# Performance work log

Measured on AMD Instinct MI355X. Metric: run time of the kernel, lower is better.

Reference implementation:

```python
import jax, jax.numpy as jnp
import numpy as np

N = 4096
E = 262144
IN_C = 128
OUT_C = 128
EDGE_D = 16


def setup_inputs() -> dict:
    key = jax.random.key(0)
    k = jax.random.split(key, 8)
    x = jax.random.normal(k[0], (N, IN_C), dtype=jnp.float32)
    edge_index = jax.random.randint(k[1], (2, E), 0, N, dtype=jnp.int64)
    edge_attr = jax.random.normal(k[2], (N, N, EDGE_D), dtype=jnp.float32)
    # nn.Linear params: y = x @ W.T + b; store pre-transposed W for x @ W
    s1 = 1.0 / np.sqrt(IN_C + EDGE_D)
    s2 = 1.0 / np.sqrt(OUT_C)
    W1 = jax.random.uniform(k[3], (IN_C + EDGE_D, OUT_C), jnp.float32, -s1, s1)
    b1 = jax.random.uniform(k[4], (OUT_C,), jnp.float32, -s1, s1)
    W2 = jax.random.uniform(k[5], (OUT_C, OUT_C), jnp.float32, -s2, s2)
    b2 = jax.random.uniform(k[6], (OUT_C,), jnp.float32, -s2, s2)
    return {"x": x, "edge_index": edge_index, "edge_attr": edge_attr,
            "W1": W1, "b1": b1, "W2": W2, "b2": b2}


def reference(x, edge_index, edge_attr, W1, b1, W2, b2):
    row, col = edge_index[0], edge_index[1]
    x_row = x[row]                      # [E, IN_C] gather
    e = edge_attr[row, col]             # [E, EDGE_D] gather from dense NxN table
    h = jnp.concatenate([x_row, e], axis=-1)     # [E, IN_C+EDGE_D]
    h = jax.nn.relu(h @ W1 + b1)                  # [E, OUT_C]
    h = jax.nn.relu(h @ W2 + b2)                  # [E, OUT_C]
    # global_add_pool(out, col): scatter-add edges into node buckets by col
    return jax.ops.segment_sum(h, col, num_segments=x.shape[0])  # [N, OUT_C]
```

## Files before the change

kernel.cpp:

```cpp
#include <hip/hip_runtime.h>
#include <hip/hip_bf16.h>

#define NN 4096
#define IC 128
#define OC 128
#define ED 16
#define EPB 64
#define NT 256
#define NSLOT 16
#define NBLK 512
#define NCPY 8

typedef __bf16 bf16x8 __attribute__((ext_vector_type(8)));
typedef float  f32x16 __attribute__((ext_vector_type(16)));

#define BAR() do { asm volatile("s_waitcnt lgkmcnt(0)" ::: "memory"); \
    __builtin_amdgcn_s_barrier(); \
    __builtin_amdgcn_sched_barrier(0); } while (0)

__device__ __forceinline__ unsigned short bf16u(float f) {
    unsigned int u = __float_as_uint(f);
    u = (u + 0x7FFFu + ((u >> 16) & 1u)) >> 16;
    return (unsigned short)u;
}
__device__ __forceinline__ float bf16tof(unsigned short h) {
    return __uint_as_float(((unsigned int)h) << 16);
}
__device__ __forceinline__ int swzk(int row) { return (row ^ (row >> 3)) & 7; }

__global__ __launch_bounds__(128) void k_xw1(
    const float* __restrict__ x, const float* __restrict__ W1,
    const float* __restrict__ b1, const int* __restrict__ eidx,
    float* __restrict__ xw1b, float* __restrict__ out,
    int* __restrict__ hist8, int E)
{
    __shared__ float xs[8][IC];
    const int t = threadIdx.x;
    const int r0 = blockIdx.x * 8;
    #pragma unroll
    for (int r = 0; r < 8; ++r) xs[r][t] = x[(size_t)(r0 + r) * IC + t];

    const float4 z = make_float4(0.f, 0.f, 0.f, 0.f);
    float4* o4 = (float4*)out;
    o4[blockIdx.x * 256 + t]       = z;
    o4[blockIdx.x * 256 + 128 + t] = z;

    {
        const int e0 = blockIdx.x * 512;
        #pragma unroll
        for (int j = 0; j < 4; ++j) {
            const int k = (2 * blockIdx.x + (j >> 1)) & (NCPY - 1);
            atomicAdd(&hist8[k * 4096 + eidx[E + e0 + t + j * 128]], 1);
        }
    }

    __syncthreads();
    float acc[8];
    const float bb = b1[t];
    #pragma unroll
    for (int r = 0; r < 8; ++r) acc[r] = bb;
    #pragma unroll 4
    for (int k = 0; k < IC; ++k) {
        const float w = W1[(size_t)k * OC + t];
        #pragma unroll
        for (int r = 0; r < 8; ++r) acc[r] = fmaf(xs[r][k], w, acc[r]);
    }
    #pragma unroll
    for (int r = 0; r < 8; ++r) xw1b[(size_t)(r0 + r) * OC + t] = acc[r];
}

__global__ __launch_bounds__(256) void k_scanA(
    const int* __restrict__ hist8, int* __restrict__ binloc,
    int* __restrict__ blocksum)
{
    __shared__ int sb[256];
    const int t = threadIdx.x;
    const int bin = blockIdx.x * 256 + t;
    int s = 0;
    #pragma unroll
    for (int k = 0; k < NCPY; ++k) s += hist8[k * 4096 + bin];
    sb[t] = s;
    __syncthreads();
    if (t == 0) {
        int a = 0;
        for (int i = 0; i < 256; ++i) { const int v = sb[i]; sb[i] = a; a += v; }
        blocksum[blockIdx.x] = a;
    }
    __syncthreads();
    binloc[bin] = sb[t];
}

__global__ __launch_bounds__(256) void k_scanB(
    const int* __restrict__ hist8, const int* __restrict__ binloc,
    const int* __restrict__ blocksum, int* __restrict__ cursor8,
    int* __restrict__ colstart, int E)
{
    __shared__ int baseL;
    const int t = threadIdx.x;
    if (t == 0) {
        int a = 0;
        for (int j = 0; j < (int)blockIdx.x; ++j) a += blocksum[j];
        baseL = a;
    }
    __syncthreads();
    const int bin = blockIdx.x * 256 + t;
    int off = baseL + binloc[bin];
    colstart[bin] = off;
    #pragma unroll
    for (int k = 0; k < NCPY; ++k) {
        cursor8[k * 4096 + bin] = off;
        off += hist8[k * 4096 + bin];
    }
    if (bin == 4095) colstart[4096] = E;
}

__global__ void k_scatter(const int* __restrict__ eidx, int* __restrict__ cursor8,
                          int2* __restrict__ csr, int E) {
    const int i = blockIdx.x * blockDim.x + threadIdx.x;
    const int k = blockIdx.x & (NCPY - 1);
    if (i < E) {
        const int row = eidx[i];
        const int col = eidx[E + i];
        const int pos = atomicAdd(&cursor8[k * 4096 + col], 1);
        csr[pos] = make_int2(row, col);
    }
}

__global__ __launch_bounds__(NT, 2) void k_edge10(
    const int2* __restrict__ csr, const float* __restrict__ eattr,
    const float* __restrict__ xw1b, const float* __restrict__ W1,
    const float* __restrict__ W2, const float* __restrict__ b2,
    const int* __restrict__ colstart, float* __restrict__ out, int E)
{
    extern __shared__ char smem[];
    char*   const h1hi = smem;
    char*   const h1lo = smem + 16384;
    float4* const eaL  = (float4*)(smem + 32768);
    float4* const w1L  = (float4*)(smem + 40960);
    float*  const lacc = (float*)(smem + 49152);
    int*    const srowL = (int*)(smem + 57344);
    int*    const scolL = srowL + 256;

    const int t   = threadIdx.x;
    const int l   = t & 63;
    const int wid = t >> 6;
    const int cg  = t & 15, eg = t >> 4;
    const int c0  = cg << 3, e0 = eg << 2;
    const int sz  = (eg >> 1) & 3;
    const int em  = t >> 2, q = t & 3;
    const int esz = (em >> 3) & 3;

    const int lm  = l & 31;
    const int hi  = l >> 5;
    const int c2  = wid * 32 + lm;

    w1L[t]       = ((const float4*)(W1 + (size_t)IC * OC))[t];
    w1L[t + NT]  = ((const float4*)(W1 + (size_t)IC * OC))[t + NT];

    bf16x8 w2h[8], w2l[8];
    #pragma unroll
    for (int s = 0; s < 8; ++s) {
        union { unsigned short us[8]; bf16x8 v; } Uh, Ul;
        #pragma unroll
        for (int j = 0; j < 8; ++j) {
            const float w = W2[(size_t)(s * 16 + hi * 8 + j) * OC + c2];
            const unsigned short h = bf16u(w);
            Uh.us[j] = h;
            Ul.us[j] = bf16u(w - bf16tof(h));
        }
        w2h[s] = Uh.v; w2l[s] = Ul.v;
    }
    const float b2s = b2[c2];

    #pragma unroll
    for (int i = 0; i < NSLOT * OC / NT; ++i) lacc[t + NT * i] = 0.f;

    const int nper = (E / EPB) / NBLK;
    const int ibb  = blockIdx.x * nper;

    if (t < EPB) {
        const int2 r0v = csr[(size_t)ibb * EPB + t];
        srowL[t] = r0v.x; scolL[t] = r0v.y;
        const int ib1 = (nper > 1) ? 1 : 0;
        const int2 r1v = csr[(size_t)(ibb + ib1) * EPB + t];
        srowL[64 + t] = r1v.x; scolL[64 + t] = r1v.y;
    }
    __syncthreads();
    const int colbase0 = scolL[0];

    float4 pA;
    {
        const int r = srowL[em], c = scolL[em];
        pA = ((const float4*)(eattr + ((size_t)r * NN + c) * ED))[q];
    }
    eaL[(em * 4 + q) ^ esz] = pA;
    float4 xa[4], xb[4];
    #pragma unroll
    for (int ri = 0; ri < 4; ++ri) {
        const int row = srowL[e0 + ri];
        const float4* p = (const float4*)(xw1b + (size_t)row * OC + c0);
        xa[ri] = p[0]; xb[ri] = p[1];
    }
    int2 pidx;
    {
        const int ib2 = (nper > 2) ? 2 : (nper - 1);
        pidx = (t < EPB) ? csr[(size_t)(ibb + ib2) * EPB + t] : make_int2(0, 0);
    }
    __syncthreads();

    for (int ii = 0; ii < nper; ++ii) {
        const int cb  = ii & 1;
        const int ib4 = ii & 3;

        float4 ha[4], hb[4];
        #pragma unroll
        for (int ri = 0; ri < 4; ++ri) { ha[ri] = xa[ri]; hb[ri] = xb[ri]; }
        #pragma unroll
        for (int dc = 0; dc < 4; ++dc) {
            float4 ev[4];
            #pragma unroll
            for (int ri = 0; ri < 4; ++ri)
                ev[ri] = eaL[cb * 256 + ((((e0 + ri) * 4 + dc)) ^ sz)];
            #pragma unroll
            for (int dd = 0; dd < 4; ++dd) {
                const int d = dc * 4 + dd;
                const float4 wA = w1L[d * 32 + cg * 2];
                const float4 wB = w1L[d * 32 + cg * 2 + 1];
                #pragma unroll
                for (int ri = 0; ri < 4; ++ri) {
                    const float evd = (dd == 0) ? ev[ri].x : (dd == 1) ? ev[ri].y
                                     : (dd == 2) ? ev[ri].z : ev[ri].w;
                    ha[ri].x = fmaf(evd, wA.x, ha[ri].x);
                    ha[ri].y = fmaf(evd, wA.y, ha[ri].y);
                    ha[ri].z = fmaf(evd, wA.z, ha[ri].z);
                    ha[ri].w = fmaf(evd, wA.w, ha[ri].w);
                    hb[ri].x = fmaf(evd, wB.x, hb[ri].x);
                    hb[ri].y = fmaf(evd, wB.y, hb[ri].y);
                    hb[ri].z = fmaf(evd, wB.z, hb[ri].z);
                    hb[ri].w = fmaf(evd, wB.w, hb[ri].w);
                }
            }
        }
        #pragma unroll
        for (int ri = 0; ri < 4; ++ri) {
            const int row = e0 + ri;
            float v[8] = { ha[ri].x, ha[ri].y, ha[ri].z, ha[ri].w,
                           hb[ri].x, hb[ri].y, hb[ri].z, hb[ri].w };
            union { unsigned short us[8]; uint4 qv; } Hh, Hl;
            #pragma unroll
            for (int j = 0; j < 8; ++j) {
                const float f = fmaxf(v[j], 0.f);
                const unsigned short h = bf16u(f);
                Hh.us[j] = h;
                Hl.us[j] = bf16u(f - bf16tof(h));
            }
            const int boff = (cg * 16) ^ (swzk(row) << 4);
            *(uint4*)(h1hi + row * 256 + boff) = Hh.qv;
            *(uint4*)(h1lo + row * 256 + boff) = Hl.qv;
        }
        if (t < EPB) {
            srowL[((ii + 2) & 3) * 64 + t] = pidx.x;
            scolL[((ii + 2) & 3) * 64 + t] = pidx.y;
        }
        {
            const int jn = (ii + 1) & 3;
            const int r = srowL[jn * 64 + em], c = scolL[jn * 64 + em];
            pA = ((const float4*)(eattr + ((size_t)r * NN + c) * ED))[q];
            #pragma unroll
            for (int ri = 0; ri < 4; ++ri) {
                const int row = srowL[jn * 64 + e0 + ri];
                const float4* p = (const float4*)(xw1b + (size_t)row * OC + c0);
                xa[ri] = p[0]; xb[ri] = p[1];
            }
        }
        {
            const int iin = (ii + 3 < nper) ? (ii + 3) : (nper - 1);
            pidx = (t < EPB) ? csr[(size_t)(ibb + iin) * EPB + t] : make_int2(0, 0);
        }
        BAR();

        f32x16 acc0 = (f32x16)(0.0f);
        f32x16 acc1 = (f32x16)(0.0f);
        const int arow0 = lm;
        const int arow1 = 32 + lm;
        const int ak0 = swzk(arow0) << 4;
        const int ak1 = swzk(arow1) << 4;
        #pragma unroll
        for (int s = 0; s < 8; ++s) {
            const int kb = s * 32 + hi * 16;
            const bf16x8 aH0 = *(const bf16x8*)(h1hi + arow0 * 256 + (kb ^ ak0));
            const bf16x8 aL0 = *(const bf16x8*)(h1lo + arow0 * 256 + (kb ^ ak0));
            const bf16x8 aH1 = *(const bf16x8*)(h1hi + arow1 * 256 + (kb ^ ak1));
            const bf16x8 aL1 = *(const bf16x8*)(h1lo + arow1 * 256 + (kb ^ ak1));
            acc0 = __builtin_amdgcn_mfma_f32_32x32x16_bf16(aH0, w2h[s], acc0, 0, 0, 0);
            acc1 = __builtin_amdgcn_mfma_f32_32x32x16_bf16(aH1, w2h[s], acc1, 0, 0, 0);
            acc0 = __builtin_amdgcn_mfma_f32_32x32x16_bf16(aL0, w2h[s], acc0, 0, 0, 0);
            acc1 = __builtin_amdgcn_mfma_f32_32x32x16_bf16(aL1, w2h[s], acc1, 0, 0, 0);
            acc0 = __builtin_amdgcn_mfma_f32_32x32x16_bf16(aH0, w2l[s], acc0, 0, 0, 0);
            acc1 = __builtin_amdgcn_mfma_f32_32x32x16_bf16(aH1, w2l[s], acc1, 0, 0, 0);
        }

        #pragma unroll
        for (int p = 0; p < 2; ++p) {
            const int mbase = p * 32 + 4 * hi;
            #pragma unroll
            for (int g = 0; g < 4; ++g) {
                const int eb = mbase + 8 * g;
                float sv;
                {
                    const float a0 = (p == 0) ? acc0[4 * g] : acc1[4 * g];
                    sv = fmaxf(a0 + b2s, 0.f);
                }
                int ccur = scolL[ib4 * 64 + eb];
                #pragma unroll
                for (int j = 1; j < 4; ++j) {
                    const float aj = (p == 0) ? acc0[4 * g + j] : acc1[4 * g + j];
                    const float v = fmaxf(aj + b2s, 0.f);
                    const int c = scolL[ib4 * 64 + eb + j];
                    if (c == ccur) {
                        sv += v;
                    } else {
                        const int slot = ccur - colbase0;
                        if (slot < NSLOT) {
                            if (sv != 0.f) atomicAdd(&lacc[slot * OC + c2], sv);
                        } else {
                            if (sv != 0.f) atomicAdd(&out[(size_t)ccur * OC + c2], sv);
                        }
                        ccur = c; sv = v;
                    }
                }
                const int slot = ccur - colbase0;
                if (slot < NSLOT) {
                    if (sv != 0.f) atomicAdd(&lacc[slot * OC + c2], sv);
                } else {
                    if (sv != 0.f) atomicAdd(&out[(size_t)ccur * OC + c2], sv);
                }
            }
        }
        eaL[(cb ^ 1) * 256 + ((em * 4 + q) ^ esz)] = pA;
        BAR();
    }

    const int blk_e0 = ibb * EPB;
    const int blk_e1 = blk_e0 + nper * EPB;
    #pragma unroll 1
    for (int s = 0; s < NSLOT; ++s) {
        const int c = colbase0 + s;
        if (c >= NN) break;
        const int cs = colstart[c];
        const int ce = colstart[c + 1];
        if (ce <= blk_e0 || cs >= blk_e1) continue;
        if (t < OC) {
            const float v = lacc[s * OC + t];
            if (cs >= blk_e0 && ce <= blk_e1) {
                out[(size_t)c * OC + t] = v;
            } else if (v != 0.f) {
                atomicAdd(&out[(size_t)c * OC + t], v);
            }
        }
    }
}

#define LDS_BYTES 59392

extern "C" void kernel_launch(void* const* d_in, const int* in_sizes, int n_in,
                              void* d_out, int out_size, void* d_ws, size_t ws_size,
                              hipStream_t stream) {
    const float* x    = (const float*)d_in[0];
    const int*   eidx = (const int*)d_in[1];
    const float* ea   = (const float*)d_in[2];
    const float* W1   = (const float*)d_in[3];
    const float* b1   = (const float*)d_in[4];
    const float* W2   = (const float*)d_in[5];
    const float* b2   = (const float*)d_in[6];
    float* out = (float*)d_out;

    const int E = in_sizes[1] / 2;

    char* ws = (char*)d_ws;
    float* xw1b     = (float*)ws;
    int*   hist8    = (int*)(ws + 2097152);
    int*   cursor8  = (int*)(ws + 2097152 + 131072);
    int*   colstart = (int*)(ws + 2097152 + 262144);
    int*   binloc   = (int*)(ws + 2097152 + 294912);
    int*   blocksum = (int*)(ws + 2097152 + 311296);
    int2*  csr      = (int2*)(ws + 2097152 + 327680);

    hipMemsetAsync(hist8, 0, 131072, stream);
    k_xw1<<<NN / 8, 128, 0, stream>>>(x, W1, b1, eidx, xw1b, out, hist8, E);
    k_scanA<<<16, 256, 0, stream>>>(hist8, binloc, blocksum);
    k_scanB<<<16, 256, 0, stream>>>(hist8, binloc, blocksum, cursor8, colstart, E);
    k_scatter<<<(E + 255) / 256, 256, 0, stream>>>(eidx, cursor8, csr, E);

    hipFuncSetAttribute(reinterpret_cast<const void*>(k_edge10),
                        hipFuncAttributeMaxDynamicSharedMemorySize, LDS_BYTES);
    k_edge10<<<NBLK, NT, LDS_BYTES, stream>>>(csr, ea, xw1b, W1, W2, b2,
                                              colstart, out, E);
}
```

Baseline: 136.9 us.

## Halve edge tile and software-pipeline layer-1 one tile ahead of MFMA layer-2

The per-block edge tile shrinks from 64 to 32 edges, and the h1 LDS buffer is double-buffered. Layer 1 (edge-attr FMA plus bf16 split) for tile i+1 now runs before layer 2's MFMA for tile i, with gathers prefetched two tiles ahead. The aim is to overlap VALU work with MFMA and cut to one barrier per iteration. The trade-off is twice as many iterations with half the work each, and only half the threads issue the edge-attr gathers.

```diff
diff --git a/kernel.cpp b/kernel.cpp
--- a/kernel.cpp
+++ b/kernel.cpp
@@ -5,7 +5,7 @@
 #define IC 128
 #define OC 128
 #define ED 16
-#define EPB 64
+#define EPB 32
 #define NT 256
 #define NSLOT 16
 #define NBLK 512
@@ -126,7 +126,7 @@
     }
 }
 
-__global__ __launch_bounds__(NT, 2) void k_edge10(
+__global__ __launch_bounds__(NT, 2) void k_edge11(
     const int2* __restrict__ csr, const float* __restrict__ eattr,
     const float* __restrict__ xw1b, const float* __restrict__ W1,
     const float* __restrict__ W2, const float* __restrict__ b2,
@@ -136,26 +136,29 @@
     char*   const h1hi = smem;
     char*   const h1lo = smem + 16384;
     float4* const eaL  = (float4*)(smem + 32768);
-    float4* const w1L  = (float4*)(smem + 40960);
-    float*  const lacc = (float*)(smem + 49152);
-    int*    const srowL = (int*)(smem + 57344);
-    int*    const scolL = srowL + 256;
+    float4* const w1L  = (float4*)(smem + 36864);
+    float*  const lacc = (float*)(smem + 45056);
+    int*    const srowL = (int*)(smem + 53248);
+    int*    const scolL = srowL + 128;
 
     const int t   = threadIdx.x;
     const int l   = t & 63;
     const int wid = t >> 6;
     const int cg  = t & 15, eg = t >> 4;
-    const int c0  = cg << 3, e0 = eg << 2;
-    const int sz  = (eg >> 1) & 3;
+    const int c0  = cg << 3, e0 = eg << 1;
+    const int sz  = (eg >> 2) & 3;
     const int em  = t >> 2, q = t & 3;
     const int esz = (em >> 3) & 3;
+    const bool gth = (t < 128);
 
     const int lm  = l & 31;
     const int hi  = l >> 5;
     const int c2  = wid * 32 + lm;
-
-    w1L[t]       = ((const float4*)(W1 + (size_t)IC * OC))[t];
-    w1L[t + NT]  = ((const float4*)(W1 + (size_t)IC * OC))[t + NT];
+    const int arow = lm;
+    const int ak  = swzk(arow) << 4;
+
+    w1L[t]      = ((const float4*)(W1 + (size_t)IC * OC))[t];
+    w1L[t + NT] = ((const float4*)(W1 + (size_t)IC * OC))[t + NT];
 
     bf16x8 w2h[8], w2l[8];
     #pragma unroll
@@ -179,165 +182,169 @@
     const int ibb  = blockIdx.x * nper;
 
     if (t < EPB) {
-        const int2 r0v = csr[(size_t)ibb * EPB + t];
-        srowL[t] = r0v.x; scolL[t] = r0v.y;
-        const int ib1 = (nper > 1) ? 1 : 0;
-        const int2 r1v = csr[(size_t)(ibb + ib1) * EPB + t];
-        srowL[64 + t] = r1v.x; scolL[64 + t] = r1v.y;
+        #pragma unroll
+        for (int b = 0; b < 3; ++b) {
+            const int ib = (b < nper) ? b : (nper - 1);
+            const int2 rc = csr[(size_t)(ibb + ib) * EPB + t];
+            srowL[b * EPB + t] = rc.x;
+            scolL[b * EPB + t] = rc.y;
+        }
     }
     __syncthreads();
     const int colbase0 = scolL[0];
 
-    float4 pA;
-    {
+    float4 pA = make_float4(0.f, 0.f, 0.f, 0.f);
+    if (gth) {
         const int r = srowL[em], c = scolL[em];
         pA = ((const float4*)(eattr + ((size_t)r * NN + c) * ED))[q];
-    }
-    eaL[(em * 4 + q) ^ esz] = pA;
-    float4 xa[4], xb[4];
-    #pragma unroll
-    for (int ri = 0; ri < 4; ++ri) {
+        eaL[(em * 4 + q) ^ esz] = pA;
+    }
+    float4 xa[2], xb[2];
+    #pragma unroll
+    for (int ri = 0; ri < 2; ++ri) {
         const int row = srowL[e0 + ri];
         const float4* p = (const float4*)(xw1b + (size_t)row * OC + c0);
         xa[ri] = p[0]; xb[ri] = p[1];
     }
+    __syncthreads();
+
+    #define LAYER1(BUF) do { \
+        float4 ha[2], hb[2]; \
+        _Pragma("unroll") \
+        for (int ri = 0; ri < 2; ++ri) { ha[ri] = xa[ri]; hb[ri] = xb[ri]; } \
+        _Pragma("unroll") \
+        for (int dc = 0; dc < 4; ++dc) { \
+            float4 ev[2]; \
+            _Pragma("unroll") \
+            for (int ri = 0; ri < 2; ++ri) \
+                ev[ri] = eaL[(BUF) * 128 + (((e0 + ri) * 4 + dc) ^ sz)]; \
+            _Pragma("unroll") \
+            for (int dd = 0; dd < 4; ++dd) { \
+                const int d = dc * 4 + dd; \
+                const float4 wA = w1L[d * 32 + cg * 2]; \
+                const float4 wB = w1L[d * 32 + cg * 2 + 1]; \
+                _Pragma("unroll") \
+                for (int ri = 0; ri < 2; ++ri) { \
+                    const float evd = (dd == 0) ? ev[ri].x : (dd == 1) ? ev[ri].y \
+                                     : (dd == 2) ? ev[ri].z : ev[ri].w; \
+                    ha[ri].x = fmaf(evd, wA.x, ha[ri].x); \
+                    ha[ri].y = fmaf(evd, wA.y, ha[ri].y); \
+                    ha[ri].z = fmaf(evd, wA.z, ha[ri].z); \
+                    ha[ri].w = fmaf(evd, wA.w, ha[ri].w); \
+                    hb[ri].x = fmaf(evd, wB.x, hb[ri].x); \
+                    hb[ri].y = fmaf(evd, wB.y, hb[ri].y); \
+                    hb[ri].z = fmaf(evd, wB.z, hb[ri].z); \
+                    hb[ri].w = fmaf(evd, wB.w, hb[ri].w); \
+                } \
+            } \
+        } \
+        _Pragma("unroll") \
+        for (int ri = 0; ri < 2; ++ri) { \
+            const int row = e0 + ri; \
+            float v[8] = { ha[ri].x, ha[ri].y, ha[ri].z, ha[ri].w, \
+                           hb[ri].x, hb[ri].y, hb[ri].z, hb[ri].w }; \
+            union { unsigned short us[8]; uint4 qv; } Hh, Hl; \
+            _Pragma("unroll") \
+            for (int j = 0; j < 8; ++j) { \
+                const float f = fmaxf(v[j], 0.f); \
+                const unsigned short h = bf16u(f); \
+                Hh.us[j] = h; \
+                Hl.us[j] = bf16u(f - bf16tof(h)); \
+            } \
+            const int boff = (cg * 16) ^ (swzk(row) << 4); \
+            *(uint4*)(h1hi + (BUF) * 8192 + row * 256 + boff) = Hh.qv; \
+            *(uint4*)(h1lo + (BUF) * 8192 + row * 256 + boff) = Hl.qv; \
+        } \
+    } while (0)
+
+    LAYER1(0);
+
+    if (gth) {
+        const int r = srowL[1 * EPB + em], c = scolL[1 * EPB + em];
+        pA = ((const float4*)(eattr + ((size_t)r * NN + c) * ED))[q];
+    }
+    #pragma unroll
+    for (int ri = 0; ri < 2; ++ri) {
+        const int row = srowL[1 * EPB + e0 + ri];
+        const float4* p = (const float4*)(xw1b + (size_t)row * OC + c0);
+        xa[ri] = p[0]; xb[ri] = p[1];
+    }
     int2 pidx;
     {
-        const int ib2 = (nper > 2) ? 2 : (nper - 1);
-        pidx = (t < EPB) ? csr[(size_t)(ibb + ib2) * EPB + t] : make_int2(0, 0);
-    }
-    __syncthreads();
+        const int ib = (3 < nper) ? 3 : (nper - 1);
+        pidx = (t < EPB) ? csr[(size_t)(ibb + ib) * EPB + t] : make_int2(0, 0);
+    }
+    if (gth) eaL[1 * 128 + ((em * 4 + q) ^ esz)] = pA;
+    BAR();
 
     for (int ii = 0; ii < nper; ++ii) {
-        const int cb  = ii & 1;
+        const int cb2 = ii & 1;
+        const int nb  = (ii + 1) & 1;
         const int ib4 = ii & 3;
 
-        float4 ha[4], hb[4];
-        #pragma unroll
-        for (int ri = 0; ri < 4; ++ri) { ha[ri] = xa[ri]; hb[ri] = xb[ri]; }
-        #pragma unroll
-        for (int dc = 0; dc < 4; ++dc) {
-            float4 ev[4];
+        if (ii + 1 < nper) LAYER1(nb);
+
+        {
+            const int jb = (ii + 2) & 3;
+            if (gth) {
+                const int r = srowL[jb * EPB + em], c = scolL[jb * EPB + em];
+                pA = ((const float4*)(eattr + ((size_t)r * NN + c) * ED))[q];
+            }
             #pragma unroll
-            for (int ri = 0; ri < 4; ++ri)
-                ev[ri] = eaL[cb * 256 + ((((e0 + ri) * 4 + dc)) ^ sz)];
-            #pragma unroll
-            for (int dd = 0; dd < 4; ++dd) {
-                const int d = dc * 4 + dd;
-                const float4 wA = w1L[d * 32 + cg * 2];
-                const float4 wB = w1L[d * 32 + cg * 2 + 1];
-                #pragma unroll
-                for (int ri = 0; ri < 4; ++ri) {
-                    const float evd = (dd == 0) ? ev[ri].x : (dd == 1) ? ev[ri].y
-                                     : (dd == 2) ? ev[ri].z : ev[ri].w;
-                    ha[ri].x = fmaf(evd, wA.x, ha[ri].x);
-                    ha[ri].y = fmaf(evd, wA.y, ha[ri].y);
-                    ha[ri].z = fmaf(evd, wA.z, ha[ri].z);
-                    ha[ri].w = fmaf(evd, wA.w, ha[ri].w);
-                    hb[ri].x = fmaf(evd, wB.x, hb[ri].x);
-                    hb[ri].y = fmaf(evd, wB.y, hb[ri].y);
-                    hb[ri].z = fmaf(evd, wB.z, hb[ri].z);
-                    hb[ri].w = fmaf(evd, wB.w, hb[ri].w);
-                }
-            }
-        }
-        #pragma unroll
-        for (int ri = 0; ri < 4; ++ri) {
-            const int row = e0 + ri;
-            float v[8] = { ha[ri].x, ha[ri].y, ha[ri].z, ha[ri].w,
-                           hb[ri].x, hb[ri].y, hb[ri].z, hb[ri].w };
-            union { unsigned short us[8]; uint4 qv; } Hh, Hl;
-            #pragma unroll
-            for (int j = 0; j < 8; ++j) {
-                const float f = fmaxf(v[j], 0.f);
-                const unsigned short h = bf16u(f);
-                Hh.us[j] = h;
-                Hl.us[j] = bf16u(f - bf16tof(h));
-            }
-            const int boff = (cg * 16) ^ (swzk(row) << 4);
-            *(uint4*)(h1hi + row * 256 + boff) = Hh.qv;
-            *(uint4*)(h1lo + row * 256 + boff) = Hl.qv;
-        }
-        if (t < EPB) {
-            srowL[((ii + 2) & 3) * 64 + t] = pidx.x;
-            scolL[((ii + 2) & 3) * 64 + t] = pidx.y;
-        }
-        {
-            const int jn = (ii + 1) & 3;
-            const int r = srowL[jn * 64 + em], c = scolL[jn * 64 + em];
-            pA = ((const float4*)(eattr + ((size_t)r * NN + c) * ED))[q];
-            #pragma unroll
-            for (int ri = 0; ri < 4; ++ri) {
-                const int row = srowL[jn * 64 + e0 + ri];
+            for (int ri = 0; ri < 2; ++ri) {
+                const int row = srowL[jb * EPB + e0 + ri];
                 const float4* p = (const float4*)(xw1b + (size_t)row * OC + c0);
                 xa[ri] = p[0]; xb[ri] = p[1];
             }
         }
+        if (t < EPB) {
+            srowL[((ii + 3) & 3) * EPB + t] = pidx.x;
+            scolL[((ii + 3) & 3) * EPB + t] = pidx.y;
+        }
         {
-            const int iin = (ii + 3 < nper) ? (ii + 3) : (nper - 1);
-            pidx = (t < EPB) ? csr[(size_t)(ibb + iin) * EPB + t] : make_int2(0, 0);
-        }
-        BAR();
-
-        f32x16 acc0 = (f32x16)(0.0f);
-        f32x16 acc1 = (f32x16)(0.0f);
-        const int arow0 = lm;
-        const int arow1 = 32 + lm;
-        const int ak0 = swzk(arow0) << 4;
-        const int ak1 = swzk(arow1) << 4;
+            const int ib = (ii + 4 < nper) ? (ii + 4) : (nper - 1);
+            pidx = (t < EPB) ? csr[(size_t)(ibb + ib) * EPB + t] : make_int2(0, 0);
+        }
+
+        f32x16 acc = (f32x16)(0.0f);
         #pragma unroll
         for (int s = 0; s < 8; ++s) {
             const int kb = s * 32 + hi * 16;
-            const bf16x8 aH0 = *(const bf16x8*)(h1hi + arow0 * 256 + (kb ^ ak0));
-            const bf16x8 aL0 = *(const bf16x8*)(h1lo + arow0 * 256 + (kb ^ ak0));
-            const bf16x8 aH1 = *(const bf16x8*)(h1hi + arow1 * 256 + (kb ^ ak1));
-            const bf16x8 aL1 = *(const bf16x8*)(h1lo + arow1 * 256 + (kb ^ ak1));
-            acc0 = __builtin_amdgcn_mfma_f32_32x32x16_bf16(aH0, w2h[s], acc0, 0, 0, 0);
-            acc1 = __builtin_amdgcn_mfma_f32_32x32x16_bf16(aH1, w2h[s], acc1, 0, 0, 0);
-            acc0 = __builtin_amdgcn_mfma_f32_32x32x16_bf16(aL0, w2h[s], acc0, 0, 0, 0);
-            acc1 = __builtin_amdgcn_mfma_f32_32x32x16_bf16(aL1, w2h[s], acc1, 0, 0, 0);
-            acc0 = __builtin_amdgcn_mfma_f32_32x32x16_bf16(aH0, w2l[s], acc0, 0, 0, 0);
-            acc1 = __builtin_amdgcn_mfma_f32_32x32x16_bf16(aH1, w2l[s], acc1, 0, 0, 0);
-        }
-
-        #pragma unroll
-        for (int p = 0; p < 2; ++p) {
-            const int mbase = p * 32 + 4 * hi;
+            const bf16x8 aH = *(const bf16x8*)(h1hi + cb2 * 8192 + arow * 256 + (kb ^ ak));
+            const bf16x8 aL = *(const bf16x8*)(h1lo + cb2 * 8192 + arow * 256 + (kb ^ ak));
+            acc = __builtin_amdgcn_mfma_f32_32x32x16_bf16(aH, w2h[s], acc, 0, 0, 0);
+            acc = __builtin_amdgcn_mfma_f32_32x32x16_bf16(aL, w2h[s], acc, 0, 0, 0);
+            acc = __builtin_amdgcn_mfma_f32_32x32x16_bf16(aH, w2l[s], acc, 0, 0, 0);
+        }
+        #pragma unroll
+        for (int g = 0; g < 4; ++g) {
+            const int eb = 4 * hi + 8 * g;
+            float sv = fmaxf(acc[4 * g] + b2s, 0.f);
+            int ccur = scolL[ib4 * EPB + eb];
             #pragma unroll
-            for (int g = 0; g < 4; ++g) {
-                const int eb = mbase + 8 * g;
-                float sv;
-                {
-                    const float a0 = (p == 0) ? acc0[4 * g] : acc1[4 * g];
-                    sv = fmaxf(a0 + b2s, 0.f);
-                }
-                int ccur = scolL[ib4 * 64 + eb];
-                #pragma unroll
-                for (int j = 1; j < 4; ++j) {
-                    const float aj = (p == 0) ? acc0[4 * g + j] : acc1[4 * g + j];
-                    const float v = fmaxf(aj + b2s, 0.f);
-                    const int c = scolL[ib4 * 64 + eb + j];
-                    if (c == ccur) {
-                        sv += v;
+            for (int j = 1; j < 4; ++j) {
+                const float v = fmaxf(acc[4 * g + j] + b2s, 0.f);
+                const int c = scolL[ib4 * EPB + eb + j];
+                if (c == ccur) {
+                    sv += v;
+                } else {
+                    const int slot = ccur - colbase0;
+                    if (slot < NSLOT) {
+                        if (sv != 0.f) atomicAdd(&lacc[slot * OC + c2], sv);
                     } else {
-                        const int slot = ccur - colbase0;
-                        if (slot < NSLOT) {
-                            if (sv != 0.f) atomicAdd(&lacc[slot * OC + c2], sv);
-                        } else {
-                            if (sv != 0.f) atomicAdd(&out[(size_t)ccur * OC + c2], sv);
-                        }
-                        ccur = c; sv = v;
+                        if (sv != 0.f) atomicAdd(&out[(size_t)ccur * OC + c2], sv);
                     }
-                }
-                const int slot = ccur - colbase0;
-                if (slot < NSLOT) {
-                    if (sv != 0.f) atomicAdd(&lacc[slot * OC + c2], sv);
-                } else {
-                    if (sv != 0.f) atomicAdd(&out[(size_t)ccur * OC + c2], sv);
+                    ccur = c; sv = v;
                 }
             }
-        }
-        eaL[(cb ^ 1) * 256 + ((em * 4 + q) ^ esz)] = pA;
+            const int slot = ccur - colbase0;
+            if (slot < NSLOT) {
+                if (sv != 0.f) atomicAdd(&lacc[slot * OC + c2], sv);
+            } else {
+                if (sv != 0.f) atomicAdd(&out[(size_t)ccur * OC + c2], sv);
+            }
+        }
+        if (gth) eaL[cb2 * 128 + ((em * 4 + q) ^ esz)] = pA;
         BAR();
     }
 
@@ -359,9 +366,10 @@
             }
         }
     }
-}
-
-#define LDS_BYTES 59392
+    #undef LAYER1
+}
+
+#define LDS_BYTES 54272
 
 extern "C" void kernel_launch(void* const* d_in, const int* in_sizes, int n_in,
                               void* d_out, int out_size, void* d_ws, size_t ws_size,
@@ -392,8 +400,8 @@
     k_scanB<<<16, 256, 0, stream>>>(hist8, binloc, blocksum, cursor8, colstart, E);
     k_scatter<<<(E + 255) / 256, 256, 0, stream>>>(eidx, cursor8, csr, E);
 
-    hipFuncSetAttribute(reinterpret_cast<const void*>(k_edge10),
+    hipFuncSetAttribute(reinterpret_cast<const void*>(k_edge11),
                         hipFuncAttributeMaxDynamicSharedMemorySize, LDS_BYTES);
-    k_edge10<<<NBLK, NT, LDS_BYTES, stream>>>(csr, ea, xw1b, W1, W2, b2,
+    k_edge11<<<NBLK, NT, LDS_BYTES, stream>>>(csr, ea, xw1b, W1, W2, b2,
                                               colstart, out, E);
 }
```

Result: slower. 142.7 us (+4.3%).

## Compute edge-attribute part of first layer with split-bf16 MFMA instead of scalar FMA

Applied to the files above, without the earlier changes.

Replaces the scalar FP32 FMA loop that applied the 16-wide edge-attribute slice of W1 with three bf16 MFMA ops using a hi/lo split for near-FP32 accuracy. The xw1b gather is loaded straight into the MFMA accumulator layout, and edge attributes go directly to registers instead of through an LDS staging buffer. This drops the eaL and w1L LDS buffers, cutting LDS use and one staging step per tile. The cost is scalar per-element gathers of xw1b (16 per accumulator) and 2-byte scattered LDS stores of h1, which may raise memory-instruction count and bank conflicts.

```diff
diff --git a/kernel.cpp b/kernel.cpp
--- a/kernel.cpp
+++ b/kernel.cpp
@@ -126,7 +126,7 @@
     }
 }
 
-__global__ __launch_bounds__(NT, 2) void k_edge10(
+__global__ __launch_bounds__(NT, 2) void k_edge12(
     const int2* __restrict__ csr, const float* __restrict__ eattr,
     const float* __restrict__ xw1b, const float* __restrict__ W1,
     const float* __restrict__ W2, const float* __restrict__ b2,
@@ -135,27 +135,16 @@
     extern __shared__ char smem[];
     char*   const h1hi = smem;
     char*   const h1lo = smem + 16384;
-    float4* const eaL  = (float4*)(smem + 32768);
-    float4* const w1L  = (float4*)(smem + 40960);
-    float*  const lacc = (float*)(smem + 49152);
-    int*    const srowL = (int*)(smem + 57344);
+    float*  const lacc = (float*)(smem + 32768);
+    int*    const srowL = (int*)(smem + 40960);
     int*    const scolL = srowL + 256;
 
     const int t   = threadIdx.x;
     const int l   = t & 63;
     const int wid = t >> 6;
-    const int cg  = t & 15, eg = t >> 4;
-    const int c0  = cg << 3, e0 = eg << 2;
-    const int sz  = (eg >> 1) & 3;
-    const int em  = t >> 2, q = t & 3;
-    const int esz = (em >> 3) & 3;
-
     const int lm  = l & 31;
     const int hi  = l >> 5;
     const int c2  = wid * 32 + lm;
-
-    w1L[t]       = ((const float4*)(W1 + (size_t)IC * OC))[t];
-    w1L[t + NT]  = ((const float4*)(W1 + (size_t)IC * OC))[t + NT];
 
     bf16x8 w2h[8], w2l[8];
     #pragma unroll
@@ -169,6 +158,18 @@
             Ul.us[j] = bf16u(w - bf16tof(h));
         }
         w2h[s] = Uh.v; w2l[s] = Ul.v;
+    }
+    bf16x8 w1h, w1l;
+    {
+        union { unsigned short us[8]; bf16x8 v; } Uh, Ul;
+        #pragma unroll
+        for (int j = 0; j < 8; ++j) {
+            const float w = W1[(size_t)(IC + hi * 8 + j) * OC + c2];
+            const unsigned short h = bf16u(w);
+            Uh.us[j] = h;
+            Ul.us[j] = bf16u(w - bf16tof(h));
+        }
+        w1h = Uh.v; w1l = Ul.v;
     }
     const float b2s = b2[c2];
 
@@ -188,156 +189,153 @@
     __syncthreads();
     const int colbase0 = scolL[0];
 
-    float4 pA;
+    float4 pe0a, pe0b, pe1a, pe1b;
     {
-        const int r = srowL[em], c = scolL[em];
-        pA = ((const float4*)(eattr + ((size_t)r * NN + c) * ED))[q];
-    }
-    eaL[(em * 4 + q) ^ esz] = pA;
-    float4 xa[4], xb[4];
-    #pragma unroll
-    for (int ri = 0; ri < 4; ++ri) {
-        const int row = srowL[e0 + ri];
-        const float4* p = (const float4*)(xw1b + (size_t)row * OC + c0);
-        xa[ri] = p[0]; xb[ri] = p[1];
+        const int r0 = srowL[lm], cc0 = scolL[lm];
+        const float* p0 = eattr + ((size_t)r0 * NN + cc0) * ED + hi * 8;
+        pe0a = ((const float4*)p0)[0]; pe0b = ((const float4*)p0)[1];
+        const int r1 = srowL[32 + lm], cc1 = scolL[32 + lm];
+        const float* p1 = eattr + ((size_t)r1 * NN + cc1) * ED + hi * 8;
+        pe1a = ((const float4*)p1)[0]; pe1b = ((const float4*)p1)[1];
     }
     int2 pidx;
     {
         const int ib2 = (nper > 2) ? 2 : (nper - 1);
         pidx = (t < EPB) ? csr[(size_t)(ibb + ib2) * EPB + t] : make_int2(0, 0);
     }
-    __syncthreads();
 
     for (int ii = 0; ii < nper; ++ii) {
-        const int cb  = ii & 1;
         const int ib4 = ii & 3;
 
-        float4 ha[4], hb[4];
-        #pragma unroll
-        for (int ri = 0; ri < 4; ++ri) { ha[ri] = xa[ri]; hb[ri] = xb[ri]; }
-        #pragma unroll
-        for (int dc = 0; dc < 4; ++dc) {
-            float4 ev[4];
-            #pragma unroll
-            for (int ri = 0; ri < 4; ++ri)
-                ev[ri] = eaL[cb * 256 + ((((e0 + ri) * 4 + dc)) ^ sz)];
-            #pragma unroll
-            for (int dd = 0; dd < 4; ++dd) {
-                const int d = dc * 4 + dd;
-                const float4 wA = w1L[d * 32 + cg * 2];
-                const float4 wB = w1L[d * 32 + cg * 2 + 1];
-                #pragma unroll
-                for (int ri = 0; ri < 4; ++ri) {
-                    const float evd = (dd == 0) ? ev[ri].x : (dd == 1) ? ev[ri].y
-                                     : (dd == 2) ? ev[ri].z : ev[ri].w;
-                    ha[ri].x = fmaf(evd, wA.x, ha[ri].x);
-                    ha[ri].y = fmaf(evd, wA.y, ha[ri].y);
-                    ha[ri].z = fmaf(evd, wA.z, ha[ri].z);
-                    ha[ri].w = fmaf(evd, wA.w, ha[ri].w);
-                    hb[ri].x = fmaf(evd, wB.x, hb[ri].x);
-                    hb[ri].y = fmaf(evd, wB.y, hb[ri].y);
-                    hb[ri].z = fmaf(evd, wB.z, hb[ri].z);
-                    hb[ri].w = fmaf(evd, wB.w, hb[ri].w);
-                }
-            }
-        }
-        #pragma unroll
-        for (int ri = 0; ri < 4; ++ri) {
-            const int row = e0 + ri;
-            float v[8] = { ha[ri].x, ha[ri].y, ha[ri].z, ha[ri].w,
-                           hb[ri].x, hb[ri].y, hb[ri].z, hb[ri].w };
-            union { unsigned short us[8]; uint4 qv; } Hh, Hl;
+        bf16x8 ah0, al0, ah1, al1;
+        {
+            const float f0[8] = { pe0a.x, pe0a.y, pe0a.z, pe0a.w,
+                                  pe0b.x, pe0b.y, pe0b.z, pe0b.w };
+            const float f1[8] = { pe1a.x, pe1a.y, pe1a.z, pe1a.w,
+                                  pe1b.x, pe1b.y, pe1b.z, pe1b.w };
+            union { unsigned short us[8]; bf16x8 v; } H0, L0, H1, L1;
             #pragma unroll
             for (int j = 0; j < 8; ++j) {
-                const float f = fmaxf(v[j], 0.f);
+                unsigned short h = bf16u(f0[j]);
+                H0.us[j] = h; L0.us[j] = bf16u(f0[j] - bf16tof(h));
+                h = bf16u(f1[j]);
+                H1.us[j] = h; L1.us[j] = bf16u(f1[j] - bf16tof(h));
+            }
+            ah0 = H0.v; al0 = L0.v; ah1 = H1.v; al1 = L1.v;
+        }
+        f32x16 acc0, acc1;
+        #pragma unroll
+        for (int reg = 0; reg < 16; ++reg) {
+            const int r = (reg & 3) + 8 * (reg >> 2) + 4 * hi;
+            acc0[reg] = xw1b[(size_t)srowL[ib4 * 64 + r] * OC + c2];
+            acc1[reg] = xw1b[(size_t)srowL[ib4 * 64 + 32 + r] * OC + c2];
+        }
+        acc0 = __builtin_amdgcn_mfma_f32_32x32x16_bf16(ah0, w1h, acc0, 0, 0, 0);
+        acc1 = __builtin_amdgcn_mfma_f32_32x32x16_bf16(ah1, w1h, acc1, 0, 0, 0);
+        acc0 = __builtin_amdgcn_mfma_f32_32x32x16_bf16(al0, w1h, acc0, 0, 0, 0);
+        acc1 = __builtin_amdgcn_mfma_f32_32x32x16_bf16(al1, w1h, acc1, 0, 0, 0);
+        acc0 = __builtin_amdgcn_mfma_f32_32x32x16_bf16(ah0, w1l, acc0, 0, 0, 0);
+        acc1 = __builtin_amdgcn_mfma_f32_32x32x16_bf16(ah1, w1l, acc1, 0, 0, 0);
+        #pragma unroll
+        for (int reg = 0; reg < 16; ++reg) {
+            const int r = (reg & 3) + 8 * (reg >> 2) + 4 * hi;
+            {
+                const float f = fmaxf(acc0[reg], 0.f);
                 const unsigned short h = bf16u(f);
-                Hh.us[j] = h;
-                Hl.us[j] = bf16u(f - bf16tof(h));
-            }
-            const int boff = (cg * 16) ^ (swzk(row) << 4);
-            *(uint4*)(h1hi + row * 256 + boff) = Hh.qv;
-            *(uint4*)(h1lo + row * 256 + boff) = Hl.qv;
+                const unsigned short lo = bf16u(f - bf16tof(h));
+                const int byt = r * 256 + ((c2 * 2) ^ (swzk(r) << 4));
+                *(unsigned short*)(h1hi + byt) = h;
+                *(unsigned short*)(h1lo + byt) = lo;
+            }
+            {
+                const int r1 = r + 32;
+                const float f = fmaxf(acc1[reg], 0.f);
+                const unsigned short h = bf16u(f);
+                const unsigned short lo = bf16u(f - bf16tof(h));
+                const int byt = r1 * 256 + ((c2 * 2) ^ (swzk(r1) << 4));
+                *(unsigned short*)(h1hi + byt) = h;
+                *(unsigned short*)(h1lo + byt) = lo;
+            }
         }
         if (t < EPB) {
             srowL[((ii + 2) & 3) * 64 + t] = pidx.x;
             scolL[((ii + 2) & 3) * 64 + t] = pidx.y;
         }
         {
-            const int jn = (ii + 1) & 3;
-            const int r = srowL[jn * 64 + em], c = scolL[jn * 64 + em];
-            pA = ((const float4*)(eattr + ((size_t)r * NN + c) * ED))[q];
-            #pragma unroll
-            for (int ri = 0; ri < 4; ++ri) {
-                const int row = srowL[jn * 64 + e0 + ri];
-                const float4* p = (const float4*)(xw1b + (size_t)row * OC + c0);
-                xa[ri] = p[0]; xb[ri] = p[1];
-            }
-        }
-        {
             const int iin = (ii + 3 < nper) ? (ii + 3) : (nper - 1);
             pidx = (t < EPB) ? csr[(size_t)(ibb + iin) * EPB + t] : make_int2(0, 0);
         }
+        {
+            const int jb = (ii + 1) & 3;
+            const int r0 = srowL[jb * 64 + lm], cc0 = scolL[jb * 64 + lm];
+            const float* p0 = eattr + ((size_t)r0 * NN + cc0) * ED + hi * 8;
+            pe0a = ((const float4*)p0)[0]; pe0b = ((const float4*)p0)[1];
+            const int r1 = srowL[jb * 64 + 32 + lm], cc1 = scolL[jb * 64 + 32 + lm];
+            const float* p1 = eattr + ((size_t)r1 * NN + cc1) * ED + hi * 8;
+            pe1a = ((const float4*)p1)[0]; pe1b = ((const float4*)p1)[1];
+        }
         BAR();
 
-        f32x16 acc0 = (f32x16)(0.0f);
-        f32x16 acc1 = (f32x16)(0.0f);
-        const int arow0 = lm;
-        const int arow1 = 32 + lm;
-        const int ak0 = swzk(arow0) << 4;
-        const int ak1 = swzk(arow1) << 4;
-        #pragma unroll
-        for (int s = 0; s < 8; ++s) {
-            const int kb = s * 32 + hi * 16;
-            const bf16x8 aH0 = *(const bf16x8*)(h1hi + arow0 * 256 + (kb ^ ak0));
-            const bf16x8 aL0 = *(const bf16x8*)(h1lo + arow0 * 256 + (kb ^ ak0));
-            const bf16x8 aH1 = *(const bf16x8*)(h1hi + arow1 * 256 + (kb ^ ak1));
-            const bf16x8 aL1 = *(const bf16x8*)(h1lo + arow1 * 256 + (kb ^ ak1));
-            acc0 = __builtin_amdgcn_mfma_f32_32x32x16_bf16(aH0, w2h[s], acc0, 0, 0, 0);
-            acc1 = __builtin_amdgcn_mfma_f32_32x32x16_bf16(aH1, w2h[s], acc1, 0, 0, 0);
-            acc0 = __builtin_amdgcn_mfma_f32_32x32x16_bf16(aL0, w2h[s], acc0, 0, 0, 0);
-            acc1 = __builtin_amdgcn_mfma_f32_32x32x16_bf16(aL1, w2h[s], acc1, 0, 0, 0);
-            acc0 = __builtin_amdgcn_mfma_f32_32x32x16_bf16(aH0, w2l[s], acc0, 0, 0, 0);
-            acc1 = __builtin_amdgcn_mfma_f32_32x32x16_bf16(aH1, w2l[s], acc1, 0, 0, 0);
-        }
-
-        #pragma unroll
-        for (int p = 0; p < 2; ++p) {
-            const int mbase = p * 32 + 4 * hi;
+        {
+            f32x16 La0 = (f32x16)(0.0f);
+            f32x16 La1 = (f32x16)(0.0f);
+            const int arow0 = lm;
+            const int arow1 = 32 + lm;
+            const int ak0 = swzk(arow0) << 4;
+            const int ak1 = swzk(arow1) << 4;
             #pragma unroll
-            for (int g = 0; g < 4; ++g) {
-                const int eb = mbase + 8 * g;
-                float sv;
-                {
-                    const float a0 = (p == 0) ? acc0[4 * g] : acc1[4 * g];
-                    sv = fmaxf(a0 + b2s, 0.f);
-                }
-                int ccur = scolL[ib4 * 64 + eb];
+            for (int s = 0; s < 8; ++s) {
+                const int kb = s * 32 + hi * 16;
+                const bf16x8 aH0 = *(const bf16x8*)(h1hi + arow0 * 256 + (kb ^ ak0));
+                const bf16x8 aL0 = *(const bf16x8*)(h1lo + arow0 * 256 + (kb ^ ak0));
+                const bf16x8 aH1 = *(const bf16x8*)(h1hi + arow1 * 256 + (kb ^ ak1));
+                const bf16x8 aL1 = *(const bf16x8*)(h1lo + arow1 * 256 + (kb ^ ak1));
+                La0 = __builtin_amdgcn_mfma_f32_32x32x16_bf16(aH0, w2h[s], La0, 0, 0, 0);
+                La1 = __builtin_amdgcn_mfma_f32_32x32x16_bf16(aH1, w2h[s], La1, 0, 0, 0);
+                La0 = __builtin_amdgcn_mfma_f32_32x32x16_bf16(aL0, w2h[s], La0, 0, 0, 0);
+                La1 = __builtin_amdgcn_mfma_f32_32x32x16_bf16(aL1, w2h[s], La1, 0, 0, 0);
+                La0 = __builtin_amdgcn_mfma_f32_32x32x16_bf16(aH0, w2l[s], La0, 0, 0, 0);
+                La1 = __builtin_amdgcn_mfma_f32_32x32x16_bf16(aH1, w2l[s], La1, 0, 0, 0);
+            }
+
+            #pragma unroll
+            for (int p = 0; p < 2; ++p) {
+                const int mbase = p * 32 + 4 * hi;
                 #pragma unroll
-                for (int j = 1; j < 4; ++j) {
-                    const float aj = (p == 0) ? acc0[4 * g + j] : acc1[4 * g + j];
-                    const float v = fmaxf(aj + b2s, 0.f);
-                    const int c = scolL[ib4 * 64 + eb + j];
-                    if (c == ccur) {
-                        sv += v;
+                for (int g = 0; g < 4; ++g) {
+                    const int eb = mbase + 8 * g;
+                    float sv;
+                    {
+                        const float a0 = (p == 0) ? La0[4 * g] : La1[4 * g];
+                        sv = fmaxf(a0 + b2s, 0.f);
+                    }
+                    int ccur = scolL[ib4 * 64 + eb];
+                    #pragma unroll
+                    for (int j = 1; j < 4; ++j) {
+                        const float aj = (p == 0) ? La0[4 * g + j] : La1[4 * g + j];
+                        const float v = fmaxf(aj + b2s, 0.f);
+                        const int c = scolL[ib4 * 64 + eb + j];
+                        if (c == ccur) {
+                            sv += v;
+                        } else {
+                            const int slot = ccur - colbase0;
+                            if (slot < NSLOT) {
+                                if (sv != 0.f) atomicAdd(&lacc[slot * OC + c2], sv);
+                            } else {
+                                if (sv != 0.f) atomicAdd(&out[(size_t)ccur * OC + c2], sv);
+                            }
+                            ccur = c; sv = v;
+                        }
+                    }
+                    const int slot = ccur - colbase0;
+                    if (slot < NSLOT) {
+                        if (sv != 0.f) atomicAdd(&lacc[slot * OC + c2], sv);
                     } else {
-                        const int slot = ccur - colbase0;
-                        if (slot < NSLOT) {
-                            if (sv != 0.f) atomicAdd(&lacc[slot * OC + c2], sv);
-                        } else {
-                            if (sv != 0.f) atomicAdd(&out[(size_t)ccur * OC + c2], sv);
-                        }
-                        ccur = c; sv = v;
+                        if (sv != 0.f) atomicAdd(&out[(size_t)ccur * OC + c2], sv);
                     }
                 }
-                const int slot = ccur - colbase0;
-                if (slot < NSLOT) {
-                    if (sv != 0.f) atomicAdd(&lacc[slot * OC + c2], sv);
-                } else {
-                    if (sv != 0.f) atomicAdd(&out[(size_t)ccur * OC + c2], sv);
-                }
-            }
-        }
-        eaL[(cb ^ 1) * 256 + ((em * 4 + q) ^ esz)] = pA;
+            }
+        }
         BAR();
     }
 
@@ -361,7 +359,7 @@
     }
 }
 
-#define LDS_BYTES 59392
+#define LDS_BYTES 43008
 
 extern "C" void kernel_launch(void* const* d_in, const int* in_sizes, int n_in,
                               void* d_out, int out_size, void* d_ws, size_t ws_size,
@@ -392,8 +390,8 @@
     k_scanB<<<16, 256, 0, stream>>>(hist8, binloc, blocksum, cursor8, colstart, E);
     k_scatter<<<(E + 255) / 256, 256, 0, stream>>>(eidx, cursor8, csr, E);
 
-    hipFuncSetAttribute(reinterpret_cast<const void*>(k_edge10),
+    hipFuncSetAttribute(reinterpret_cast<const void*>(k_edge12),
                         hipFuncAttributeMaxDynamicSharedMemorySize, LDS_BYTES);
-    k_edge10<<<NBLK, NT, LDS_BYTES, stream>>>(csr, ea, xw1b, W1, W2, b2,
+    k_edge12<<<NBLK, NT, LDS_BYTES, stream>>>(csr, ea, xw1b, W1, W2, b2,
                                               colstart, out, E);
 }
```

Result: faster. 132.0 us (-3.6%).
